# Kernel tuning notes

Hardware: AMD Instinct MI355X
Metric: run time of the kernel (lower is better)

The kernel has to match this reference:

```python
import jax, jax.numpy as jnp
import numpy as np

B, S = 1024, 512
V, E, H, T = 50000, 300, 800, 50


def setup_inputs() -> dict:
    key = jax.random.key(0)
    ks = jax.random.split(key, 8)
    ids = jax.random.randint(ks[0], (B, S), 0, V, dtype=jnp.int64 if jax.config.jax_enable_x64 else jnp.int32)
    return {
        "ids": ids,
        "rho": jax.random.normal(ks[1], (V, E), jnp.float32) * 0.02,
        "alpha": jax.random.normal(ks[2], (T, E), jnp.float32) * 0.02,
        "W1": jax.random.normal(ks[3], (E, H), jnp.float32) * 0.05,
        "b1": jnp.zeros((H,), jnp.float32),
        "Wmu": jax.random.normal(ks[4], (H, T), jnp.float32) * 0.05,
        "bmu": jnp.zeros((T,), jnp.float32),
        "Wlv": jax.random.normal(ks[5], (H, T), jnp.float32) * 0.05,
        "blv": jnp.zeros((T,), jnp.float32),
    }


def reference(ids, rho, alpha, W1, b1, Wmu, bmu, Wlv, blv):
    b, s = ids.shape
    v = rho.shape[0]
    # bag-of-words histogram: scatter-add instead of dense one_hot+reduce_sum
    bows = jnp.zeros((b, v), rho.dtype).at[jnp.arange(b)[:, None], ids].add(1.0)
    # zero out special tokens 1 and 2 (original: x * (1 - sum(one_hot([1,2]))))
    bows = bows.at[:, jnp.array([1, 2])].set(0.0)
    normal_bows = bows / jnp.sum(bows, axis=-1, keepdims=True)
    # encoder (eval mode: dropout is identity)
    x = jnp.einsum('bv,ve->be', normal_bows, rho)
    h = jax.nn.relu(x @ W1 + b1)
    mu_theta = h @ Wmu + bmu
    logsigma_theta = h @ Wlv + blv
    kl_theta = -0.5 * jnp.sum(1.0 + logsigma_theta - mu_theta**2 - jnp.exp(logsigma_theta), axis=-1)
    # reparameterize (eval/inference mode): z = mu
    theta = jax.nn.softmax(mu_theta, axis=-1)  # [B, T]
    beta = jax.nn.softmax(jnp.einsum('te,ve->tv', alpha, rho), axis=-1)  # [T, V]
    lookup = jnp.log(theta @ beta + 1e-5)  # [B, V]
    recon_loss = -jnp.sum(lookup * bows, axis=-1)
    loss = jnp.mean(recon_loss) + jnp.mean(kl_theta)
    return theta, loss
```

## Files before the change

### kernel.cpp

```cpp
#include <hip/hip_runtime.h>
#include <math.h>


#define Bn 1024
#define Sn 512
#define Vn 50000
#define En 300
#define Hn 800
#define Tn 50
#define KP 320
#define BSTR 64
#define W1FRAG_N (50 * 10 * 64 * 8)
#define WFRAG_N  (8 * 25 * 64 * 8)
#define NRANGE 8
#define VRANGE (Vn / NRANGE)
#define CASTB (Vn * (KP / 4) / 256)
#define K4B (Vn / 16)

typedef __bf16 bf16x8 __attribute__((ext_vector_type(8)));
typedef float  f32x4  __attribute__((ext_vector_type(4)));

__device__ __forceinline__ float waveReduceSum(float v) {
    #pragma unroll
    for (int off = 32; off > 0; off >>= 1) v += __shfl_xor(v, off, 64);
    return v;
}
__device__ __forceinline__ float waveReduceMax(float v) {
    #pragma unroll
    for (int off = 32; off > 0; off >>= 1) v = fmaxf(v, __shfl_xor(v, off, 64));
    return v;
}
__device__ __forceinline__ unsigned short f2bf(float x) {
    unsigned u = __float_as_uint(x);
    return (unsigned short)((u + 0x7FFFu + ((u >> 16) & 1u)) >> 16);
}
__device__ __forceinline__ float bf_lo(unsigned u) { return __uint_as_float(u << 16); }
__device__ __forceinline__ float bf_hi(unsigned u) { return __uint_as_float(u & 0xFFFF0000u); }
__device__ __forceinline__ int lane_prefix(unsigned long long m) {
    return __builtin_amdgcn_mbcnt_hi((unsigned)(m >> 32),
           __builtin_amdgcn_mbcnt_lo((unsigned)m, 0));
}

__global__ __launch_bounds__(256) void ka_init(
        const float4* __restrict__ rho4, ushort4* __restrict__ rhoh4,
        const float* __restrict__ alpha, const float* __restrict__ W1,
        const float* __restrict__ Wmu, const float* __restrict__ Wlv,
        unsigned short* __restrict__ bfrag, unsigned short* __restrict__ w1frag,
        unsigned short* __restrict__ wfrag, float* __restrict__ topicsumR,
        float* __restrict__ loss, float* __restrict__ xbar) {
    if (blockIdx.x < CASTB) {
        const int i = blockIdx.x * 256 + threadIdx.x;
        int v = i / (KP / 4), s = i - v * (KP / 4);
        ushort4 p = {0, 0, 0, 0};
        if (s < En / 4) {
            float4 r = rho4[v * (En / 4) + s];
            p.x = f2bf(r.x); p.y = f2bf(r.y); p.z = f2bf(r.z); p.w = f2bf(r.w);
        }
        rhoh4[i] = p;
        return;
    }
    const int gid = (blockIdx.x - CASTB) * 256 + threadIdx.x;
    if (gid < 512) topicsumR[gid] = 0.f;
    if (gid == 520) *loss = 0.f;
    if (gid < Bn * En) xbar[gid] = 0.f;
    if (gid < 4 * 10 * 64 * 8) {
        int j = gid & 7;
        int lane = (gid >> 3) & 63;
        int rest = gid >> 9;
        int kt = rest % 10, w = rest / 10;
        int t = 16 * w + (lane & 15);
        int e = kt * 32 + (lane >> 4) * 8 + j;
        bfrag[gid] = (t < Tn && e < En) ? f2bf(alpha[t * En + e]) : (unsigned short)0;
    }
    if (gid < W1FRAG_N) {
        int j = gid & 7, lane = (gid >> 3) & 63, rest = gid >> 9;
        int kt = rest % 10, nt = rest / 10;
        int e = kt * 32 + (lane >> 4) * 8 + j;
        int hcol = nt * 16 + (lane & 15);
        w1frag[gid] = (e < En) ? f2bf(W1[e * Hn + hcol]) : (unsigned short)0;
    } else {
        int g2 = gid - W1FRAG_N;
        if (g2 < WFRAG_N) {
            int j = g2 & 7, lane = (g2 >> 3) & 63, rest = g2 >> 9;
            int kt = rest % 25, nt = rest / 25;
            int k = kt * 32 + (lane >> 4) * 8 + j;
            int t = (nt & 3) * 16 + (lane & 15);
            float val = 0.f;
            if (t < Tn) val = (nt < 4) ? Wmu[k * Tn + t] : Wlv[k * Tn + t];
            wfrag[g2] = f2bf(val);
        }
    }
}

__global__ __launch_bounds__(256) void kb_beta_tokens(
        const unsigned short* __restrict__ rhoh,
        const unsigned short* __restrict__ bfrag,
        unsigned int* __restrict__ betaU32, float* __restrict__ topicsumR,
        const int* __restrict__ ids, int* __restrict__ toks,
        int* __restrict__ cnt, float* __restrict__ xbar) {
    __shared__ unsigned short trans[16 * 66];
    __shared__ __align__(16) int sid[Sn];
    __shared__ int sfid[Sn];
    __shared__ int scount, sfull;
    const int tid = threadIdx.x;

    if (blockIdx.x < K4B) {
        const int wave = tid >> 6, lane = tid & 63;
        const int quad = lane >> 4, l15 = lane & 15;
        const int v0 = blockIdx.x * 16;
        const unsigned short* arow = rhoh + (size_t)(v0 + l15) * KP + quad * 8;
        f32x4 acc = {0.f, 0.f, 0.f, 0.f};
        #pragma unroll
        for (int kt = 0; kt < 10; ++kt) {
            bf16x8 a = *(const bf16x8*)(arow + kt * 32);
            bf16x8 bv = *(const bf16x8*)(bfrag + ((wave * 10 + kt) * 64 + lane) * 8);
            acc = __builtin_amdgcn_mfma_f32_16x16x32_bf16(a, bv, acc, 0, 0, 0);
        }
        float ts = 0.f;
        #pragma unroll
        for (int r = 0; r < 4; ++r) {
            float ev = expf(acc[r]);
            ts += ev;
            trans[(quad * 4 + r) * 66 + 16 * wave + l15] = f2bf(ev);
        }
        ts += __shfl_xor(ts, 16, 64);
        ts += __shfl_xor(ts, 32, 64);
        const int t = 16 * wave + l15;
        if (lane < 16 && t < Tn)
            atomicAdd(&topicsumR[(blockIdx.x & 7) * 64 + t], ts);
        __syncthreads();
        unsigned int* dst = betaU32 + (size_t)v0 * 32;
        const unsigned int* tr32 = (const unsigned int*)trans;
        for (int i = tid; i < 16 * 32; i += 256)
            dst[i] = tr32[(i >> 5) * 33 + (i & 31)];
        return;
    }
    const int blk = blockIdx.x - K4B;
    const int r = blk & (NRANGE - 1), b = blk >> 3;
    const int lo = r * VRANGE, hi = lo + VRANGE;
    const int lane = tid & 63;
    if (tid == 0) { scount = 0; sfull = 0; }
    __syncthreads();
    #pragma unroll
    for (int s0 = 0; s0 < Sn; s0 += 256) {
        int id = ids[b * Sn + s0 + tid];
        bool val = (id != 1 && id != 2);
        bool inr = val && id >= lo && id < hi;
        unsigned long long mb = __ballot(inr);
        int pre = lane_prefix(mb);
        int wc = __popcll(mb);
        int base = 0;
        if (lane == 0 && wc) base = atomicAdd(&scount, wc);
        base = __shfl(base, 0, 64);
        if (inr) sid[base + pre] = id;
        if (r == 0) {
            unsigned long long fb = __ballot(val);
            int fpre = lane_prefix(fb);
            int fwc = __popcll(fb);
            int fbase = 0;
            if (lane == 0 && fwc) fbase = atomicAdd(&sfull, fwc);
            fbase = __shfl(fbase, 0, 64);
            if (val) sfid[fbase + fpre] = id;
        }
    }
    __syncthreads();
    if (r == 0) {
        const int nf = sfull;
        for (int i = tid; i < nf; i += 256) toks[b * Sn + i] = sfid[i];
        if (tid == 0) cnt[b] = nf;
    }
    const int m = scount;
    const unsigned int* rhoh32 = (const unsigned int*)rhoh;
    if (tid < En / 2 && m > 0) {
        float ax = 0.f, ay = 0.f;
        int s = 0;
        for (; s + 8 <= m; s += 8) {
            const int4 q0 = *(const int4*)&sid[s];
            const int4 q1 = *(const int4*)&sid[s + 4];
            unsigned u0 = rhoh32[q0.x * (KP / 2) + tid];
            unsigned u1 = rhoh32[q0.y * (KP / 2) + tid];
            unsigned u2 = rhoh32[q0.z * (KP / 2) + tid];
            unsigned u3 = rhoh32[q0.w * (KP / 2) + tid];
            unsigned u4 = rhoh32[q1.x * (KP / 2) + tid];
            unsigned u5 = rhoh32[q1.y * (KP / 2) + tid];
            unsigned u6 = rhoh32[q1.z * (KP / 2) + tid];
            unsigned u7 = rhoh32[q1.w * (KP / 2) + tid];
            ax += bf_lo(u0); ay += bf_hi(u0);
            ax += bf_lo(u1); ay += bf_hi(u1);
            ax += bf_lo(u2); ay += bf_hi(u2);
            ax += bf_lo(u3); ay += bf_hi(u3);
            ax += bf_lo(u4); ay += bf_hi(u4);
            ax += bf_lo(u5); ay += bf_hi(u5);
            ax += bf_lo(u6); ay += bf_hi(u6);
            ax += bf_lo(u7); ay += bf_hi(u7);
        }
        for (; s < m; ++s) {
            unsigned u = rhoh32[sid[s] * (KP / 2) + tid];
            ax += bf_lo(u); ay += bf_hi(u);
        }
        atomicAdd(&xbar[b * En + 2 * tid], ax);
        atomicAdd(&xbar[b * En + 2 * tid + 1], ay);
    }
}

__global__ __launch_bounds__(256) void k2m_h(
        const float* __restrict__ xbar, const int* __restrict__ cnt,
        const unsigned short* __restrict__ w1frag,
        const float* __restrict__ b1, unsigned short* __restrict__ hbh) {
    __shared__ unsigned short xs[16 * 328];
    __shared__ float invn[16];
    const int tid = threadIdx.x;
    const int wave = tid >> 6, lane = tid & 63;
    const int quad = lane >> 4, l15 = lane & 15;
    const int b0 = blockIdx.x * 16;
    if (tid < 16) invn[tid] = 1.0f / (float)cnt[b0 + tid];
    __syncthreads();
    for (int i = tid; i < 16 * KP; i += 256) {
        int row = i / KP, e = i - row * KP;
        xs[row * 328 + e] = (e < En) ? f2bf(xbar[(b0 + row) * En + e] * invn[row])
                                     : (unsigned short)0;
    }
    __syncthreads();
    const int nt = blockIdx.y * 4 + wave;
    if (nt < 50) {
        const unsigned short* arow = xs + l15 * 328 + quad * 8;
        f32x4 acc = {0.f, 0.f, 0.f, 0.f};
        #pragma unroll
        for (int kt = 0; kt < 10; ++kt) {
            bf16x8 a = *(const bf16x8*)(arow + kt * 32);
            bf16x8 bv = *(const bf16x8*)(w1frag + ((size_t)(nt * 10 + kt) * 64 + lane) * 8);
            acc = __builtin_amdgcn_mfma_f32_16x16x32_bf16(a, bv, acc, 0, 0, 0);
        }
        const int col = nt * 16 + l15;
        const float bias = b1[col];
        #pragma unroll
        for (int r = 0; r < 4; ++r) {
            int row = b0 + quad * 4 + r;
            hbh[(size_t)row * Hn + col] = f2bf(fmaxf(acc[r] + bias, 0.f));
        }
    }
}

__global__ __launch_bounds__(256) void k3_theta(
        const unsigned short* __restrict__ hbh,
        const unsigned short* __restrict__ wfrag,
        const float* __restrict__ bmu, const float* __restrict__ blv,
        float* __restrict__ theta, float* __restrict__ loss) {
    __shared__ float mlds[16 * 65];
    __shared__ float llds[16 * 65];
    const int tid = threadIdx.x;
    const int wave = tid >> 6, lane = tid & 63;
    const int quad = lane >> 4, l15 = lane & 15;
    const int b0 = blockIdx.x * 16;
    const unsigned short* arow = hbh + (size_t)(b0 + l15) * Hn + quad * 8;
    f32x4 am = {0.f, 0.f, 0.f, 0.f}, al = {0.f, 0.f, 0.f, 0.f};
    #pragma unroll
    for (int kt = 0; kt < 25; ++kt) {
        bf16x8 a  = *(const bf16x8*)(arow + kt * 32);
        bf16x8 bm = *(const bf16x8*)(wfrag + ((size_t)(wave * 25 + kt) * 64 + lane) * 8);
        bf16x8 bl = *(const bf16x8*)(wfrag + ((size_t)((4 + wave) * 25 + kt) * 64 + lane) * 8);
        am = __builtin_amdgcn_mfma_f32_16x16x32_bf16(a, bm, am, 0, 0, 0);
        al = __builtin_amdgcn_mfma_f32_16x16x32_bf16(a, bl, al, 0, 0, 0);
    }
    const int t = wave * 16 + l15;
    const float bm_ = (t < Tn) ? bmu[t] : 0.f;
    const float bl_ = (t < Tn) ? blv[t] : 0.f;
    #pragma unroll
    for (int r = 0; r < 4; ++r) {
        int row = quad * 4 + r;
        mlds[row * 65 + t] = am[r] + bm_;
        llds[row * 65 + t] = al[r] + bl_;
    }
    __syncthreads();
    const int tt = (lane < Tn) ? lane : (Tn - 1);
    const bool act = (lane < Tn);
    float klacc = 0.f;
    #pragma unroll
    for (int k = 0; k < 4; ++k) {
        int row = wave * 4 + k;
        float mu = mlds[row * 65 + tt];
        float lv = llds[row * 65 + tt];
        float m = waveReduceMax(act ? mu : -1e30f);
        float ex = act ? expf(mu - m) : 0.f;
        float ssum = waveReduceSum(ex);
        if (act) theta[(b0 + row) * Tn + lane] = ex / ssum;
        klacc += waveReduceSum(act ? (1.f + lv - mu * mu - expf(lv)) : 0.f);
    }
    if (lane == 0) atomicAdd(loss, -0.5f * klacc * (1.0f / (float)Bn));
}

__global__ __launch_bounds__(256) void k6_recon(
        const int* __restrict__ toks, const int* __restrict__ cnt,
        const float* __restrict__ theta, const float* __restrict__ topicsumR,
        const unsigned short* __restrict__ betaUh, float* __restrict__ loss) {
    __shared__ float sw[Tn];
    __shared__ float swred[4];
    const int b = blockIdx.x, tid = threadIdx.x;
    if (tid < Tn) {
        float z = 0.f;
        #pragma unroll
        for (int j = 0; j < 8; ++j) z += topicsumR[j * 64 + tid];
        sw[tid] = theta[b * Tn + tid] / z;
    }
    __syncthreads();
    float wr[Tn];
    #pragma unroll
    for (int t = 0; t < Tn; ++t) wr[t] = sw[t];
    float lsum = 0.f;
    const int n = cnt[b];
    for (int i = tid; i < n; i += 256) {
        int v = toks[b * Sn + i];
        const uint4* q = (const uint4*)(betaUh + (size_t)v * BSTR);
        float dot = 0.f;
        #pragma unroll
        for (int k = 0; k < 6; ++k) {
            uint4 u = q[k];
            int t = 8 * k;
            dot += wr[t]     * bf_lo(u.x) + wr[t + 1] * bf_hi(u.x);
            dot += wr[t + 2] * bf_lo(u.y) + wr[t + 3] * bf_hi(u.y);
            dot += wr[t + 4] * bf_lo(u.z) + wr[t + 5] * bf_hi(u.z);
            dot += wr[t + 6] * bf_lo(u.w) + wr[t + 7] * bf_hi(u.w);
        }
        unsigned d = ((const unsigned*)q)[24];
        dot += wr[48] * bf_lo(d) + wr[49] * bf_hi(d);
        lsum += logf(dot + 1e-5f);
    }
    float s = waveReduceSum(lsum);
    const int wave = tid >> 6, lane = tid & 63;
    if (lane == 0) swred[wave] = s;
    __syncthreads();
    if (tid == 0) {
        float tot = swred[0] + swred[1] + swred[2] + swred[3];
        atomicAdd(loss, -tot * (1.0f / (float)Bn));
    }
}

extern "C" void kernel_launch(void* const* d_in, const int* in_sizes, int n_in,
                              void* d_out, int out_size, void* d_ws, size_t ws_size,
                              hipStream_t stream) {
    const int*   ids   = (const int*)d_in[0];
    const float* rho   = (const float*)d_in[1];
    const float* alpha = (const float*)d_in[2];
    const float* W1    = (const float*)d_in[3];
    const float* b1    = (const float*)d_in[4];
    const float* Wmu   = (const float*)d_in[5];
    const float* bmu   = (const float*)d_in[6];
    const float* Wlv   = (const float*)d_in[7];
    const float* blv   = (const float*)d_in[8];

    float* theta = (float*)d_out;
    float* loss  = theta + Bn * Tn;

    char* w = (char*)d_ws;
    float* topicsumR = (float*)w;               w += 8 * 64 * 4;
    unsigned short* bfrag = (unsigned short*)w; w += 4 * 10 * 64 * 8 * 2;
    unsigned short* w1frag = (unsigned short*)w; w += (size_t)W1FRAG_N * 2;
    unsigned short* wfrag = (unsigned short*)w;  w += (size_t)WFRAG_N * 2;
    int*   cnt      = (int*)w;                  w += Bn * 4;
    int*   toks     = (int*)w;                  w += Bn * Sn * 4;
    float* xbar     = (float*)w;                w += Bn * En * 4;
    unsigned short* hbh = (unsigned short*)w;   w += (size_t)Bn * Hn * 2;
    unsigned short* rhoh = (unsigned short*)w;  w += (size_t)Vn * KP * 2;
    unsigned int* betaU32 = (unsigned int*)w;   w += (size_t)Vn * 128;

    const int k0grid = (W1FRAG_N + WFRAG_N + 255) / 256;
    ka_init<<<CASTB + k0grid, 256, 0, stream>>>(
        (const float4*)rho, (ushort4*)rhoh, alpha, W1, Wmu, Wlv,
        bfrag, w1frag, wfrag, topicsumR, loss, xbar);
    kb_beta_tokens<<<K4B + Bn * NRANGE, 256, 0, stream>>>(
        rhoh, bfrag, betaU32, topicsumR, ids, toks, cnt, xbar);
    k2m_h<<<dim3(64, 13), 256, 0, stream>>>(xbar, cnt, w1frag, b1, hbh);
    k3_theta<<<64, 256, 0, stream>>>(hbh, wfrag, bmu, blv, theta, loss);
    k6_recon<<<Bn, 256, 0, stream>>>(toks, cnt, theta, topicsumR,
                                     (const unsigned short*)betaU32, loss);
}
```

Before: 210.4 us.

## Gather rho rows with 16-byte loads across all waves and store per-range partial sums

The per-document embedding gather now runs on all four waves, with each lane loading a uint4 (8 bf16 values) per token row instead of only 150 threads loading 4 bytes each. Each block reduces its waves' results in shared memory and writes one partial vector per (document, vocab range), replacing global float atomics into xbar. Because of this the xbar zero-initialisation in the init kernel is dropped, and the next kernel sums the 8 range partials with float4 loads. The cost is a larger workspace and more global traffic when the partials are read back, and lanes 40-63 sit idle during the gather.

```diff
diff --git a/kernel.cpp b/kernel.cpp
--- a/kernel.cpp
+++ b/kernel.cpp
@@ -41,13 +41,18 @@
            __builtin_amdgcn_mbcnt_lo((unsigned)m, 0));
 }
 
+#define ACC8(u) { a0 += bf_lo((u).x); a1 += bf_hi((u).x); \
+                  a2 += bf_lo((u).y); a3 += bf_hi((u).y); \
+                  a4 += bf_lo((u).z); a5 += bf_hi((u).z); \
+                  a6 += bf_lo((u).w); a7 += bf_hi((u).w); }
+
 __global__ __launch_bounds__(256) void ka_init(
         const float4* __restrict__ rho4, ushort4* __restrict__ rhoh4,
         const float* __restrict__ alpha, const float* __restrict__ W1,
         const float* __restrict__ Wmu, const float* __restrict__ Wlv,
         unsigned short* __restrict__ bfrag, unsigned short* __restrict__ w1frag,
         unsigned short* __restrict__ wfrag, float* __restrict__ topicsumR,
-        float* __restrict__ loss, float* __restrict__ xbar) {
+        float* __restrict__ loss) {
     if (blockIdx.x < CASTB) {
         const int i = blockIdx.x * 256 + threadIdx.x;
         int v = i / (KP / 4), s = i - v * (KP / 4);
@@ -62,7 +67,6 @@
     const int gid = (blockIdx.x - CASTB) * 256 + threadIdx.x;
     if (gid < 512) topicsumR[gid] = 0.f;
     if (gid == 520) *loss = 0.f;
-    if (gid < Bn * En) xbar[gid] = 0.f;
     if (gid < 4 * 10 * 64 * 8) {
         int j = gid & 7;
         int lane = (gid >> 3) & 63;
@@ -97,15 +101,16 @@
         const unsigned short* __restrict__ bfrag,
         unsigned int* __restrict__ betaU32, float* __restrict__ topicsumR,
         const int* __restrict__ ids, int* __restrict__ toks,
-        int* __restrict__ cnt, float* __restrict__ xbar) {
+        int* __restrict__ cnt, float* __restrict__ xbarP) {
     __shared__ unsigned short trans[16 * 66];
     __shared__ __align__(16) int sid[Sn];
     __shared__ int sfid[Sn];
+    __shared__ float xred[4][320];
     __shared__ int scount, sfull;
     const int tid = threadIdx.x;
+    const int wave = tid >> 6, lane = tid & 63;
 
     if (blockIdx.x < K4B) {
-        const int wave = tid >> 6, lane = tid & 63;
         const int quad = lane >> 4, l15 = lane & 15;
         const int v0 = blockIdx.x * 16;
         const unsigned short* arow = rhoh + (size_t)(v0 + l15) * KP + quad * 8;
@@ -138,7 +143,6 @@
     const int blk = blockIdx.x - K4B;
     const int r = blk & (NRANGE - 1), b = blk >> 3;
     const int lo = r * VRANGE, hi = lo + VRANGE;
-    const int lane = tid & 63;
     if (tid == 0) { scount = 0; sfull = 0; }
     __syncthreads();
     #pragma unroll
@@ -170,41 +174,35 @@
         if (tid == 0) cnt[b] = nf;
     }
     const int m = scount;
-    const unsigned int* rhoh32 = (const unsigned int*)rhoh;
-    if (tid < En / 2 && m > 0) {
-        float ax = 0.f, ay = 0.f;
-        int s = 0;
-        for (; s + 8 <= m; s += 8) {
-            const int4 q0 = *(const int4*)&sid[s];
-            const int4 q1 = *(const int4*)&sid[s + 4];
-            unsigned u0 = rhoh32[q0.x * (KP / 2) + tid];
-            unsigned u1 = rhoh32[q0.y * (KP / 2) + tid];
-            unsigned u2 = rhoh32[q0.z * (KP / 2) + tid];
-            unsigned u3 = rhoh32[q0.w * (KP / 2) + tid];
-            unsigned u4 = rhoh32[q1.x * (KP / 2) + tid];
-            unsigned u5 = rhoh32[q1.y * (KP / 2) + tid];
-            unsigned u6 = rhoh32[q1.z * (KP / 2) + tid];
-            unsigned u7 = rhoh32[q1.w * (KP / 2) + tid];
-            ax += bf_lo(u0); ay += bf_hi(u0);
-            ax += bf_lo(u1); ay += bf_hi(u1);
-            ax += bf_lo(u2); ay += bf_hi(u2);
-            ax += bf_lo(u3); ay += bf_hi(u3);
-            ax += bf_lo(u4); ay += bf_hi(u4);
-            ax += bf_lo(u5); ay += bf_hi(u5);
-            ax += bf_lo(u6); ay += bf_hi(u6);
-            ax += bf_lo(u7); ay += bf_hi(u7);
-        }
-        for (; s < m; ++s) {
-            unsigned u = rhoh32[sid[s] * (KP / 2) + tid];
-            ax += bf_lo(u); ay += bf_hi(u);
-        }
-        atomicAdd(&xbar[b * En + 2 * tid], ax);
-        atomicAdd(&xbar[b * En + 2 * tid + 1], ay);
-    }
+    float a0 = 0.f, a1 = 0.f, a2 = 0.f, a3 = 0.f;
+    float a4 = 0.f, a5 = 0.f, a6 = 0.f, a7 = 0.f;
+    if (lane < 40) {
+        const uint4* rb = (const uint4*)rhoh;
+        int s = wave;
+        for (; s + 12 < m; s += 16) {
+            int i0 = sid[s], i1 = sid[s + 4], i2 = sid[s + 8], i3 = sid[s + 12];
+            uint4 u0 = rb[(size_t)i0 * 40 + lane];
+            uint4 u1 = rb[(size_t)i1 * 40 + lane];
+            uint4 u2 = rb[(size_t)i2 * 40 + lane];
+            uint4 u3 = rb[(size_t)i3 * 40 + lane];
+            ACC8(u0); ACC8(u1); ACC8(u2); ACC8(u3);
+        }
+        for (; s < m; s += 4) {
+            uint4 u = rb[(size_t)sid[s] * 40 + lane];
+            ACC8(u);
+        }
+        float* xw = &xred[wave][lane * 8];
+        xw[0] = a0; xw[1] = a1; xw[2] = a2; xw[3] = a3;
+        xw[4] = a4; xw[5] = a5; xw[6] = a6; xw[7] = a7;
+    }
+    __syncthreads();
+    float* xbp = xbarP + ((size_t)b * NRANGE + r) * KP;
+    for (int c = tid; c < KP; c += 256)
+        xbp[c] = xred[0][c] + xred[1][c] + xred[2][c] + xred[3][c];
 }
 
 __global__ __launch_bounds__(256) void k2m_h(
-        const float* __restrict__ xbar, const int* __restrict__ cnt,
+        const float* __restrict__ xbarP, const int* __restrict__ cnt,
         const unsigned short* __restrict__ w1frag,
         const float* __restrict__ b1, unsigned short* __restrict__ hbh) {
     __shared__ unsigned short xs[16 * 328];
@@ -215,10 +213,20 @@
     const int b0 = blockIdx.x * 16;
     if (tid < 16) invn[tid] = 1.0f / (float)cnt[b0 + tid];
     __syncthreads();
-    for (int i = tid; i < 16 * KP; i += 256) {
-        int row = i / KP, e = i - row * KP;
-        xs[row * 328 + e] = (e < En) ? f2bf(xbar[(b0 + row) * En + e] * invn[row])
-                                     : (unsigned short)0;
+    for (int i = tid; i < 16 * (KP / 4); i += 256) {
+        int row = i / (KP / 4), e4 = (i - row * (KP / 4)) * 4;
+        const float* bp = xbarP + ((size_t)(b0 + row) * NRANGE) * KP + e4;
+        float sx = 0.f, sy = 0.f, sz = 0.f, sw_ = 0.f;
+        #pragma unroll
+        for (int rr = 0; rr < NRANGE; ++rr) {
+            float4 v = *(const float4*)(bp + rr * KP);
+            sx += v.x; sy += v.y; sz += v.z; sw_ += v.w;
+        }
+        float in = invn[row];
+        ushort4 o;
+        o.x = f2bf(sx * in); o.y = f2bf(sy * in);
+        o.z = f2bf(sz * in); o.w = f2bf(sw_ * in);
+        *(ushort4*)&xs[row * 328 + e4] = o;
     }
     __syncthreads();
     const int nt = blockIdx.y * 4 + wave;
@@ -358,7 +366,7 @@
     unsigned short* wfrag = (unsigned short*)w;  w += (size_t)WFRAG_N * 2;
     int*   cnt      = (int*)w;                  w += Bn * 4;
     int*   toks     = (int*)w;                  w += Bn * Sn * 4;
-    float* xbar     = (float*)w;                w += Bn * En * 4;
+    float* xbarP    = (float*)w;                w += (size_t)Bn * NRANGE * KP * 4;
     unsigned short* hbh = (unsigned short*)w;   w += (size_t)Bn * Hn * 2;
     unsigned short* rhoh = (unsigned short*)w;  w += (size_t)Vn * KP * 2;
     unsigned int* betaU32 = (unsigned int*)w;   w += (size_t)Vn * 128;
@@ -366,10 +374,10 @@
     const int k0grid = (W1FRAG_N + WFRAG_N + 255) / 256;
     ka_init<<<CASTB + k0grid, 256, 0, stream>>>(
         (const float4*)rho, (ushort4*)rhoh, alpha, W1, Wmu, Wlv,
-        bfrag, w1frag, wfrag, topicsumR, loss, xbar);
+        bfrag, w1frag, wfrag, topicsumR, loss);
     kb_beta_tokens<<<K4B + Bn * NRANGE, 256, 0, stream>>>(
-        rhoh, bfrag, betaU32, topicsumR, ids, toks, cnt, xbar);
-    k2m_h<<<dim3(64, 13), 256, 0, stream>>>(xbar, cnt, w1frag, b1, hbh);
+        rhoh, bfrag, betaU32, topicsumR, ids, toks, cnt, xbarP);
+    k2m_h<<<dim3(64, 13), 256, 0, stream>>>(xbarP, cnt, w1frag, b1, hbh);
     k3_theta<<<64, 256, 0, stream>>>(hbh, wfrag, bmu, blv, theta, loss);
     k6_recon<<<Bn, 256, 0, stream>>>(toks, cnt, theta, topicsumR,
                                      (const unsigned short*)betaU32, loss);
```

New measurement: 200.4 us. -4.8%, faster.
